# Kernel optimization log

Hardware: AMD Instinct MI355X
Metric: run time of the kernel (lower is better)

The kernel has to match this reference:

```python
import jax, jax.numpy as jnp
from jax import lax
import numpy as np

HIDDEN = 128
SEQ = 784
IN = 1
OUT = 10
BATCH = 1024


def setup_inputs() -> dict:
    key = jax.random.key(0)
    ks = jax.random.split(key, 7)
    s_i = 1.0 / np.sqrt(HIDDEN)
    x = jax.random.normal(ks[0], (BATCH, SEQ, IN), dtype=jnp.float32)
    Wi = jax.random.uniform(ks[1], (3 * HIDDEN, IN), jnp.float32, -s_i, s_i)
    bi = jax.random.uniform(ks[2], (3 * HIDDEN,), jnp.float32, -s_i, s_i)
    Wh = jax.random.uniform(ks[3], (3 * HIDDEN, HIDDEN), jnp.float32, -s_i, s_i)
    bh = jax.random.uniform(ks[4], (3 * HIDDEN,), jnp.float32, -s_i, s_i)
    Wfc = jax.random.uniform(ks[5], (OUT, HIDDEN), jnp.float32, -s_i, s_i)
    bfc = jax.random.uniform(ks[6], (OUT,), jnp.float32, -s_i, s_i)
    return {"x": x, "Wi": Wi, "bi": bi, "Wh": Wh, "bh": bh, "Wfc": Wfc, "bfc": bfc}


def reference(x, Wi, bi, Wh, bh, Wfc, bfc):
    # Precompute all input projections at once: [b, T, 3H]
    xi = jnp.einsum('bti,gi->btg', x, Wi) + bi
    xi_t = jnp.swapaxes(xi, 0, 1)  # [T, b, 3H] for scan over time

    def step(h, xt):
        gh = h @ Wh.T + bh                     # [b, 3H]
        ir, iz, inn = jnp.split(xt, 3, axis=-1)
        hr, hz, hn = jnp.split(gh, 3, axis=-1)
        r = jax.nn.sigmoid(ir + hr)
        z = jax.nn.sigmoid(iz + hz)
        n = jnp.tanh(inn + r * hn)
        h_new = (1.0 - z) * n + z * h
        return h_new, None

    h0 = jnp.zeros((x.shape[0], Wh.shape[1]), dtype=x.dtype)
    h, _ = lax.scan(step, h0, xi_t)
    logits = h @ Wfc.T + bfc                   # [b, 10]
    return logits
```

## Files before the change

### kernel.cpp

```cpp
#include <hip/hip_runtime.h>
#include <hip/hip_bf16.h>

#define SEQ_T 784
#define HID   128
#define S_H   160

typedef __attribute__((ext_vector_type(8))) short  short8;
typedef __attribute__((ext_vector_type(4))) float  floatx4;
typedef __attribute__((ext_vector_type(8))) float  float8;

static __device__ __forceinline__ short bf16_of(float f) {
  union { float f; unsigned u; } v; v.f = f;
  return (short)((v.u + 0x7fffu + ((v.u >> 16) & 1u)) >> 16);
}

#define MFMA_BF16 __builtin_amdgcn_mfma_f32_16x16x32_bf16

extern "C" __global__ void __launch_bounds__(512, 2)
gru_sparse4_t(const float* __restrict__ x,
              const float* __restrict__ Wi,
              const float* __restrict__ bi,
              const float* __restrict__ Wh,
              const float* __restrict__ bh,
              const float* __restrict__ Wfc,
              const float* __restrict__ bfc,
              float* __restrict__ out)
{
  const int tid  = threadIdx.x;
  const int wv   = tid >> 6;
  const int lane = tid & 63;
  const int quad = lane >> 4;
  const int nn   = lane & 15;
  const int j    = (wv << 4) | nn;
  const int b0   = blockIdx.x * 4;

  __shared__ __align__(16) float xs[SEQ_T][4];
  __shared__ __align__(16) short hb[2][4 * S_H];
  __shared__ float hfin[4][HID];

  for (int i = tid; i < 2 * 4 * S_H; i += 512) ((short*)hb)[i] = 0;
  for (int i = tid; i < 4 * SEQ_T; i += 512) {
    const int r = i / SEQ_T;
    const int t = i - r * SEQ_T;
    xs[t][r] = x[(size_t)(b0 + r) * SEQ_T + t];
  }

  const float wi_r = Wi[j],  wi_z = Wi[HID + j],  wi_n = Wi[2 * HID + j];
  const float c_r  = bi[j] + bh[j];
  const float c_z  = bi[HID + j] + bh[HID + j];
  const float bi_n = bi[2 * HID + j];
  const float bh_n = bh[2 * HID + j];

  short8 whi[3][4];
  #pragma unroll
  for (int g = 0; g < 3; ++g) {
    const float* wrow = Wh + (size_t)(g * HID + j) * HID;
    #pragma unroll
    for (int kk = 0; kk < 4; ++kk) {
      float8 w = *(const float8*)(wrow + kk * 32 + quad * 8);
      short8 hi;
      #pragma unroll
      for (int e = 0; e < 8; ++e) hi[e] = bf16_of(w[e]);
      whi[g][kk] = hi;
    }
  }

  float h = 0.0f;
  const bool rlane = ((nn & 3) == 0);
  const int a_off  = (nn >> 2) * S_H + quad * 8;
  const int w_off  = quad * S_H + j;
  const bool wlane = ((nn & 1) == 0);

  __syncthreads();

  const floatx4 Z = {0.f, 0.f, 0.f, 0.f};

  short8 ah0 = {0,0,0,0,0,0,0,0}, ah1 = ah0, ah2 = ah0, ah3 = ah0;

  auto step = [&](const short* __restrict__ hc, short* __restrict__ nx,
                  float xt) {
    if (rlane) {
      ah0 = *(const short8*)(hc + a_off);
      ah1 = *(const short8*)(hc + a_off + 32);
      ah2 = *(const short8*)(hc + a_off + 64);
      ah3 = *(const short8*)(hc + a_off + 96);
    }

    __builtin_amdgcn_s_setprio(1);
    floatx4 r0 = MFMA_BF16(ah0, whi[0][0], Z, 0, 0, 0);
    floatx4 r1 = MFMA_BF16(ah1, whi[0][1], Z, 0, 0, 0);
    floatx4 z0 = MFMA_BF16(ah0, whi[1][0], Z, 0, 0, 0);
    floatx4 z1 = MFMA_BF16(ah1, whi[1][1], Z, 0, 0, 0);
    floatx4 n0 = MFMA_BF16(ah0, whi[2][0], Z, 0, 0, 0);
    floatx4 n1 = MFMA_BF16(ah1, whi[2][1], Z, 0, 0, 0);
    r0 = MFMA_BF16(ah2, whi[0][2], r0, 0, 0, 0);
    r1 = MFMA_BF16(ah3, whi[0][3], r1, 0, 0, 0);
    z0 = MFMA_BF16(ah2, whi[1][2], z0, 0, 0, 0);
    z1 = MFMA_BF16(ah3, whi[1][3], z1, 0, 0, 0);
    n0 = MFMA_BF16(ah2, whi[2][2], n0, 0, 0, 0);
    n1 = MFMA_BF16(ah3, whi[2][3], n1, 0, 0, 0);
    __builtin_amdgcn_s_setprio(0);

    const float pr = fmaf(xt, wi_r, c_r) + (r0[0] + r1[0]);
    const float pz = fmaf(xt, wi_z, c_z) + (z0[0] + z1[0]);
    const float rg = __builtin_amdgcn_rcpf(1.0f + __expf(-pr));
    const float zg = __builtin_amdgcn_rcpf(1.0f + __expf(-pz));
    const float pn = fmaf(rg, (n0[0] + n1[0]) + bh_n, fmaf(xt, wi_n, bi_n));
    const float ng = 1.0f - 2.0f * __builtin_amdgcn_rcpf(1.0f + __expf(2.0f * pn));
    h = fmaf(zg, h - ng, ng);

    const float hnb = __int_as_float(
        __builtin_amdgcn_mov_dpp(__float_as_int(h), 0xB1, 0xF, 0xF, true));
    int hp;
    asm("v_cvt_pk_bf16_f32 %0, %1, %2" : "=v"(hp) : "v"(h), "v"(hnb));
    if (wlane) *(int*)(nx + w_off) = hp;
  };

  for (int t = 0; t < SEQ_T; t += 2) {
    const float xa = xs[t][quad];
    const float xb = xs[t + 1][quad];
    step(hb[0], hb[1], xa);
    __syncthreads();
    step(hb[1], hb[0], xb);
    __syncthreads();
  }

  hfin[quad][j] = h;
  __syncthreads();
  if (tid < 40) {
    const int r = tid / 10, o = tid - r * 10;
    float acc = bfc[o];
    #pragma unroll 4
    for (int k = 0; k < HID; ++k)
      acc = fmaf(hfin[r][k], Wfc[o * HID + k], acc);
    out[(size_t)(b0 + r) * 10 + o] = acc;
  }
}

extern "C" void kernel_launch(void* const* d_in, const int* in_sizes, int n_in,
                              void* d_out, int out_size, void* d_ws, size_t ws_size,
                              hipStream_t stream) {
  const float* x   = (const float*)d_in[0];
  const float* Wi  = (const float*)d_in[1];
  const float* bi  = (const float*)d_in[2];
  const float* Wh  = (const float*)d_in[3];
  const float* bh  = (const float*)d_in[4];
  const float* Wfc = (const float*)d_in[5];
  const float* bfc = (const float*)d_in[6];
  hipLaunchKernelGGL(gru_sparse4_t, dim3(256), dim3(512), 0, stream,
                     x, Wi, bi, Wh, bh, Wfc, bfc, (float*)d_out);
}
```

Before: 325.4 us.

## Use int8 MFMA for reset/update gates, keep bf16 for candidate gate

The r and z gate recurrent matmuls are quantized to int8, with per-row weight scales and hidden state scaled by 127, and computed with the 16x16x64 i8 MFMA. This halves the MFMA count for those gates, while the n gate stays in bf16. A second int8 copy of h is written to LDS each step. Sigmoid/tanh constants are prefolded with log2e so the gates use exp2 directly. The change risks accuracy loss from int8 quantization of h and the weights.

```diff
diff --git a/kernel.cpp b/kernel.cpp
--- a/kernel.cpp
+++ b/kernel.cpp
@@ -1,12 +1,13 @@
 #include <hip/hip_runtime.h>
-#include <hip/hip_bf16.h>
 
 #define SEQ_T 784
 #define HID   128
 #define S_H   160
+#define SB    320
 
 typedef __attribute__((ext_vector_type(8))) short  short8;
 typedef __attribute__((ext_vector_type(4))) float  floatx4;
+typedef __attribute__((ext_vector_type(4))) int    intx4;
 typedef __attribute__((ext_vector_type(8))) float  float8;
 
 static __device__ __forceinline__ short bf16_of(float f) {
@@ -15,16 +16,17 @@
 }
 
 #define MFMA_BF16 __builtin_amdgcn_mfma_f32_16x16x32_bf16
+#define MFMA_I8   __builtin_amdgcn_mfma_i32_16x16x64_i8
 
 extern "C" __global__ void __launch_bounds__(512, 2)
-gru_sparse4_t(const float* __restrict__ x,
-              const float* __restrict__ Wi,
-              const float* __restrict__ bi,
-              const float* __restrict__ Wh,
-              const float* __restrict__ bh,
-              const float* __restrict__ Wfc,
-              const float* __restrict__ bfc,
-              float* __restrict__ out)
+gru_hyb_t(const float* __restrict__ x,
+          const float* __restrict__ Wi,
+          const float* __restrict__ bi,
+          const float* __restrict__ Wh,
+          const float* __restrict__ bh,
+          const float* __restrict__ Wfc,
+          const float* __restrict__ bfc,
+          float* __restrict__ out)
 {
   const int tid  = threadIdx.x;
   const int wv   = tid >> 6;
@@ -35,93 +37,134 @@
   const int b0   = blockIdx.x * 4;
 
   __shared__ __align__(16) float xs[SEQ_T][4];
-  __shared__ __align__(16) short hb[2][4 * S_H];
+  __shared__ __align__(16) short hbf[2][4 * S_H];
+  __shared__ __align__(16) char  hq [2][4 * SB];
   __shared__ float hfin[4][HID];
 
-  for (int i = tid; i < 2 * 4 * S_H; i += 512) ((short*)hb)[i] = 0;
+  for (int i = tid; i < 2 * 4 * S_H; i += 512) ((short*)hbf)[i] = 0;
+  for (int i = tid; i < 2 * 4 * SB / 4; i += 512) ((int*)hq)[i] = 0;
   for (int i = tid; i < 4 * SEQ_T; i += 512) {
     const int r = i / SEQ_T;
     const int t = i - r * SEQ_T;
     xs[t][r] = x[(size_t)(b0 + r) * SEQ_T + t];
   }
 
-  const float wi_r = Wi[j],  wi_z = Wi[HID + j],  wi_n = Wi[2 * HID + j];
-  const float c_r  = bi[j] + bh[j];
-  const float c_z  = bi[HID + j] + bh[HID + j];
-  const float bi_n = bi[2 * HID + j];
-  const float bh_n = bh[2 * HID + j];
+  const float LOG2E = 1.4426950408889634f;
+  const float TL2E  = 2.0f * LOG2E;
 
-  short8 whi[3][4];
-  #pragma unroll
-  for (int g = 0; g < 3; ++g) {
-    const float* wrow = Wh + (size_t)(g * HID + j) * HID;
+  const float wi_rn = -Wi[j] * LOG2E;
+  const float c_rn  = -(bi[j] + bh[j]) * LOG2E;
+  const float wi_zn = -Wi[HID + j] * LOG2E;
+  const float c_zn  = -(bi[HID + j] + bh[HID + j]) * LOG2E;
+  const float win2  = Wi[2 * HID + j] * TL2E;
+  const float bin2  = bi[2 * HID + j] * TL2E;
+  const float bhn2  = bh[2 * HID + j] * TL2E;
+
+  short8 whn[4];
+  {
+    const float* wrow = Wh + (size_t)(2 * HID + j) * HID;
     #pragma unroll
     for (int kk = 0; kk < 4; ++kk) {
       float8 w = *(const float8*)(wrow + kk * 32 + quad * 8);
       short8 hi;
       #pragma unroll
       for (int e = 0; e < 8; ++e) hi[e] = bf16_of(w[e]);
-      whi[g][kk] = hi;
+      whn[kk] = hi;
     }
   }
 
+  intx4 wq[2][2];
+  float d_rn, d_zn;
+  #pragma unroll
+  for (int g = 0; g < 2; ++g) {
+    const float* wrow = Wh + (size_t)(g * HID + j) * HID;
+    float m = 0.0f;
+    #pragma unroll
+    for (int k8 = 0; k8 < 16; ++k8) {
+      float8 w = *(const float8*)(wrow + k8 * 8);
+      #pragma unroll
+      for (int e = 0; e < 8; ++e) m = fmaxf(m, fabsf(w[e]));
+    }
+    const float inv = 127.0f / m;
+    #pragma unroll
+    for (int kk = 0; kk < 2; ++kk) {
+      int dw[4] = {0, 0, 0, 0};
+      #pragma unroll
+      for (int e = 0; e < 16; ++e) {
+        const int q = (int)rintf(wrow[kk * 64 + quad * 16 + e] * inv) & 0xFF;
+        dw[e >> 2] |= q << (8 * (e & 3));
+      }
+      intx4 v = {dw[0], dw[1], dw[2], dw[3]};
+      wq[g][kk] = v;
+    }
+    const float d = -m * (1.0f / 16129.0f) * LOG2E;
+    if (g == 0) d_rn = d; else d_zn = d;
+  }
+
   float h = 0.0f;
-  const bool rlane = ((nn & 3) == 0);
-  const int a_off  = (nn >> 2) * S_H + quad * 8;
-  const int w_off  = quad * S_H + j;
-  const bool wlane = ((nn & 1) == 0);
+  const bool rlane  = ((nn & 3) == 0);
+  const int abf_off = (nn >> 2) * S_H + quad * 8;
+  const int aq_off  = (nn >> 2) * SB + quad * 16;
+  const int wbf_off = quad * S_H + j;
+  const int wq_off  = quad * SB + j;
+  const bool wlane  = ((nn & 1) == 0);
 
   __syncthreads();
 
-  const floatx4 Z = {0.f, 0.f, 0.f, 0.f};
+  const floatx4 Zf = {0.f, 0.f, 0.f, 0.f};
+  const intx4   Zi = {0, 0, 0, 0};
+  short8 ah0 = {0,0,0,0,0,0,0,0}, ah1 = ah0, ah2 = ah0, ah3 = ah0;
+  intx4  a0 = Zi, a1 = Zi;
 
-  short8 ah0 = {0,0,0,0,0,0,0,0}, ah1 = ah0, ah2 = ah0, ah3 = ah0;
-
-  auto step = [&](const short* __restrict__ hc, short* __restrict__ nx,
-                  float xt) {
+  auto step = [&](const short* __restrict__ bc, const char* __restrict__ qc,
+                  short* __restrict__ bn, char* __restrict__ qn, float xt) {
     if (rlane) {
-      ah0 = *(const short8*)(hc + a_off);
-      ah1 = *(const short8*)(hc + a_off + 32);
-      ah2 = *(const short8*)(hc + a_off + 64);
-      ah3 = *(const short8*)(hc + a_off + 96);
+      ah0 = *(const short8*)(bc + abf_off);
+      ah1 = *(const short8*)(bc + abf_off + 32);
+      ah2 = *(const short8*)(bc + abf_off + 64);
+      ah3 = *(const short8*)(bc + abf_off + 96);
+      a0  = *(const intx4*)(qc + aq_off);
+      a1  = *(const intx4*)(qc + aq_off + 64);
     }
+    const float wrc = fmaf(xt, wi_rn, c_rn);
+    const float wzc = fmaf(xt, wi_zn, c_zn);
+    const float u   = fmaf(xt, win2, bin2);
 
     __builtin_amdgcn_s_setprio(1);
-    floatx4 r0 = MFMA_BF16(ah0, whi[0][0], Z, 0, 0, 0);
-    floatx4 r1 = MFMA_BF16(ah1, whi[0][1], Z, 0, 0, 0);
-    floatx4 z0 = MFMA_BF16(ah0, whi[1][0], Z, 0, 0, 0);
-    floatx4 z1 = MFMA_BF16(ah1, whi[1][1], Z, 0, 0, 0);
-    floatx4 n0 = MFMA_BF16(ah0, whi[2][0], Z, 0, 0, 0);
-    floatx4 n1 = MFMA_BF16(ah1, whi[2][1], Z, 0, 0, 0);
-    r0 = MFMA_BF16(ah2, whi[0][2], r0, 0, 0, 0);
-    r1 = MFMA_BF16(ah3, whi[0][3], r1, 0, 0, 0);
-    z0 = MFMA_BF16(ah2, whi[1][2], z0, 0, 0, 0);
-    z1 = MFMA_BF16(ah3, whi[1][3], z1, 0, 0, 0);
-    n0 = MFMA_BF16(ah2, whi[2][2], n0, 0, 0, 0);
-    n1 = MFMA_BF16(ah3, whi[2][3], n1, 0, 0, 0);
+    intx4   cr = MFMA_I8(a0, wq[0][0], Zi, 0, 0, 0);
+    intx4   cz = MFMA_I8(a0, wq[1][0], Zi, 0, 0, 0);
+    floatx4 n0 = MFMA_BF16(ah0, whn[0], Zf, 0, 0, 0);
+    floatx4 n1 = MFMA_BF16(ah1, whn[1], Zf, 0, 0, 0);
+    cr = MFMA_I8(a1, wq[0][1], cr, 0, 0, 0);
+    cz = MFMA_I8(a1, wq[1][1], cz, 0, 0, 0);
+    n0 = MFMA_BF16(ah2, whn[2], n0, 0, 0, 0);
+    n1 = MFMA_BF16(ah3, whn[3], n1, 0, 0, 0);
     __builtin_amdgcn_s_setprio(0);
 
-    const float pr = fmaf(xt, wi_r, c_r) + (r0[0] + r1[0]);
-    const float pz = fmaf(xt, wi_z, c_z) + (z0[0] + z1[0]);
-    const float rg = __builtin_amdgcn_rcpf(1.0f + __expf(-pr));
-    const float zg = __builtin_amdgcn_rcpf(1.0f + __expf(-pz));
-    const float pn = fmaf(rg, (n0[0] + n1[0]) + bh_n, fmaf(xt, wi_n, bi_n));
-    const float ng = 1.0f - 2.0f * __builtin_amdgcn_rcpf(1.0f + __expf(2.0f * pn));
+    const float rg = __builtin_amdgcn_rcpf(
+        1.0f + __builtin_amdgcn_exp2f(fmaf((float)cr[0], d_rn, wrc)));
+    const float zg = __builtin_amdgcn_rcpf(
+        1.0f + __builtin_amdgcn_exp2f(fmaf((float)cz[0], d_zn, wzc)));
+    const float nsum = n0[0] + n1[0];
+    const float t  = fmaf(rg, fmaf(TL2E, nsum, bhn2), u);
+    const float ng = fmaf(-2.0f, __builtin_amdgcn_rcpf(
+        1.0f + __builtin_amdgcn_exp2f(t)), 1.0f);
     h = fmaf(zg, h - ng, ng);
 
     const float hnb = __int_as_float(
         __builtin_amdgcn_mov_dpp(__float_as_int(h), 0xB1, 0xF, 0xF, true));
     int hp;
     asm("v_cvt_pk_bf16_f32 %0, %1, %2" : "=v"(hp) : "v"(h), "v"(hnb));
-    if (wlane) *(int*)(nx + w_off) = hp;
+    if (wlane) *(int*)(bn + wbf_off) = hp;
+    qn[wq_off] = (char)(int)rintf(h * 127.0f);
   };
 
   for (int t = 0; t < SEQ_T; t += 2) {
     const float xa = xs[t][quad];
     const float xb = xs[t + 1][quad];
-    step(hb[0], hb[1], xa);
+    step(hbf[0], hq[0], hbf[1], hq[1], xa);
     __syncthreads();
-    step(hb[1], hb[0], xb);
+    step(hbf[1], hq[1], hbf[0], hq[0], xb);
     __syncthreads();
   }
 
@@ -147,6 +190,6 @@
   const float* bh  = (const float*)d_in[4];
   const float* Wfc = (const float*)d_in[5];
   const float* bfc = (const float*)d_in[6];
-  hipLaunchKernelGGL(gru_sparse4_t, dim3(256), dim3(512), 0, stream,
+  hipLaunchKernelGGL(gru_hyb_t, dim3(256), dim3(512), 0, stream,
                      x, Wi, bi, Wh, bh, Wfc, bfc, (float*)d_out);
 }
```

Result: slower. 344.7 us (+5.9%).
